# Optimization experiments

Hardware: AMD Instinct MI355X
Metric: run time of the kernel (lower is better)

The kernel has to match this reference:

```python
import jax, jax.numpy as jnp
import numpy as np

B, V, T, D, NC = 512, 4, 16, 512, 174
EPS = 1e-5
_edges = np.ones((V, V)) - np.eye(V)
SEND = np.where(_edges)[0]   # [12]
RECV = np.where(_edges)[1]   # [12]
E2N = jnp.asarray(np.eye(V)[RECV].T, dtype=jnp.float32)  # [V, E] one-hot recv matrix


def _bn(x, g, b):
    # BatchNorm1d in training mode: batch stats over flattened rows, biased var
    m = x.mean(axis=0)
    v = jnp.var(x, axis=0)
    return (x - m) * jax.lax.rsqrt(v + EPS) * g + b


def _mlp(x, w1, b1, w2, b2, g, bb):
    # RefNRIMLP: Linear-ELU-(Dropout p=0.1 disabled/eval)-Linear-ELU-BN
    h = jax.nn.elu(x @ w1 + b1)
    h = jax.nn.elu(h @ w2 + b2)
    return _bn(h, g, bb)


def setup_inputs() -> dict:
    key = jax.random.key(0)
    ks = iter(jax.random.split(key, 64))
    def W(*s):
        return jax.random.normal(next(ks), s, dtype=jnp.float32) * 0.02
    def zeros(*s):
        return jnp.zeros(s, jnp.float32)
    def ones(*s):
        return jnp.ones(s, jnp.float32)
    return dict(
        global_img_input=zeros(1),
        box_categories=jax.random.randint(next(ks), (B, T, V), 0, 3),
        box_input=jax.random.uniform(next(ks), (B, T, V, 4), dtype=jnp.float32),
        hand_id=jax.random.randint(next(ks), (B,), 0, 2),
        video_label=jax.random.randint(next(ks), (B,), 0, NC),
        emb=W(3, D // 2),
        c2f_w1=W(4, D // 2), c2f_g1=ones(D // 2), c2f_b1=zeros(D // 2),
        c2f_w2=W(D // 2, D), c2f_g2=ones(D), c2f_b2=zeros(D),
        fus_w=W(D + D // 2, D), fus_g=ones(D), fus_b=zeros(D),
        m1_w1=W(2 * D, D), m1_b1=zeros(D), m1_w2=W(D, D), m1_b2=zeros(D), m1_g=ones(D), m1_bb=zeros(D),
        m2_w1=W(D, D), m2_b1=zeros(D), m2_w2=W(D, D), m2_b2=zeros(D), m2_g=ones(D), m2_bb=zeros(D),
        t1_w1=W(2 * D, D), t1_b1=zeros(D), t1_w2=W(D, D), t1_b2=zeros(D), t1_g=ones(D), t1_bb=zeros(D),
        ps_w1=W(D, D), ps_g1=ones(D), ps_b1=zeros(D), ps_w2=W(D, D), ps_g2=ones(D), ps_b2=zeros(D),
        tb_w1=W(T * D, D), tb_g1=ones(D), tb_b1=zeros(D), tb_w2=W(D, D), tb_g2=ones(D), tb_b2=zeros(D),
        cl_w1=W(D, D), cl_b1=zeros(D), cl_w2=W(D, 512), cl_b2=zeros(512),
        cl_w3=W(512, NC), cl_b3=zeros(NC),
    )


def reference(global_img_input, box_categories, box_input, hand_id, video_label,
              emb, c2f_w1, c2f_g1, c2f_b1, c2f_w2, c2f_g2, c2f_b2,
              fus_w, fus_g, fus_b,
              m1_w1, m1_b1, m1_w2, m1_b2, m1_g, m1_bb,
              m2_w1, m2_b1, m2_w2, m2_b2, m2_g, m2_bb,
              t1_w1, t1_b1, t1_w2, t1_b2, t1_g, t1_bb,
              ps_w1, ps_g1, ps_b1, ps_w2, ps_g2, ps_b2,
              tb_w1, tb_g1, tb_b1, tb_w2, tb_g2, tb_b2,
              cl_w1, cl_b1, cl_w2, cl_b2, cl_w3, cl_b3):
    b = hand_id.shape[0]
    # [b,T,V,*] -> [b,V,T,*] -> flatten rows
    x = box_input.transpose(0, 2, 1, 3).reshape(-1, 4)          # [b*V*T, 4]
    cats = box_categories.transpose(0, 2, 1).reshape(-1)        # [b*V*T]
    pad_mask = (jnp.arange(3)[:, None] != 0).astype(emb.dtype)  # padding_idx=0
    ce = (emb * pad_mask)[cats]                                 # [b*V*T, D/2]
    # coord_to_feature: Linear(no bias)-BN-ReLU x2
    h = jax.nn.relu(_bn(x @ c2f_w1, c2f_g1, c2f_b1))
    h = jax.nn.relu(_bn(h @ c2f_w2, c2f_g2, c2f_b2))
    # coord_category_fusion
    bf = jax.nn.relu(_bn(jnp.concatenate([h, ce], axis=1) @ fus_w, fus_g, fus_b))
    bf = bf.reshape(b, V, T, D)
    # node2edge gather + mlp1
    e = jnp.concatenate([bf[:, SEND], bf[:, RECV]], axis=-1).reshape(-1, 2 * D)
    e = _mlp(e, m1_w1, m1_b1, m1_w2, m1_b2, m1_g, m1_bb).reshape(b, len(SEND), T, D)
    # edge2node: one-hot matmul aggregation / (V-1)
    n = jnp.einsum('ve,betd->bvtd', E2N, e) / (V - 1)
    n = _mlp(n.reshape(-1, D), m2_w1, m2_b1, m2_w2, m2_b2, m2_g, m2_bb).reshape(b, V, T, D)
    # temporal MLP on cat(node, bf)
    p = jnp.concatenate([n, bf], axis=-1).reshape(-1, 2 * D)
    p = _mlp(p, t1_w1, t1_b1, t1_w2, t1_b2, t1_g, t1_bb)
    # point_spatial_node_fusion
    p = jax.nn.relu(_bn(p @ ps_w1, ps_g1, ps_b1))
    p = jax.nn.relu(_bn(p @ ps_w2, ps_g2, ps_b2))
    # t_box_feature_fusion over flattened time
    q = p.reshape(b * V, T * D)
    q = jax.nn.relu(_bn(q @ tb_w1, tb_g1, tb_b1))
    q = jax.nn.relu(_bn(q @ tb_w2, tb_g2, tb_b2))
    feat = q.reshape(b, V, D).mean(axis=1)                      # mean over boxes
    h1 = jax.nn.relu(feat @ cl_w1 + cl_b1)
    h2 = jax.nn.relu(h1 @ cl_w2 + cl_b2)
    pf = h2 @ cl_w3 + cl_b3                                      # [b, NC]
    return (pf, video_label)
```

## Files before the change

kernel.cpp:

```cpp
#include <hip/hip_runtime.h>
#include <math.h>

#define EPS_ 1e-5f

static constexpr int Bb = 512, Vv = 4, Tt = 16, Dd = 512, NCc = 174;
static constexpr int NROW = Bb * Vv * Tt;
static constexpr int EROW = Bb * 12 * Tt;
static constexpr int CB = 128;
static constexpr int NCHUNK = Bb / CB;
static constexpr int CROWS_N = CB * Vv * Tt;
static constexpr int CROWS_E = CB * 12 * Tt;

__constant__ int d_SEND[12] = {0,0,0,1,1,1,2,2,2,3,3,3};
__constant__ int d_RECV[12] = {1,2,3,0,2,3,0,1,3,0,1,2};
__constant__ int d_EOFV[4][3] = {{3,6,9},{0,7,10},{1,4,11},{2,5,8}};

typedef float f32x4 __attribute__((ext_vector_type(4)));
typedef short s16x8 __attribute__((ext_vector_type(8)));

static __device__ __forceinline__ float b2f(unsigned short u) {
    union { unsigned int i; float f; } x; x.i = ((unsigned int)u) << 16; return x.f;
}
static __device__ __forceinline__ unsigned short f2b(float f) {
    union { float f; unsigned int i; } x; x.f = f;
    unsigned int r = (x.i + 0x7fffu + ((x.i >> 16) & 1u)) >> 16;
    return (unsigned short)r;
}
static __device__ __forceinline__ float act_f(float v, int act) {
    if (act == 1) return fmaxf(v, 0.f);
    if (act == 2) return (v > 0.f) ? v : (__expf(v) - 1.f);
    return v;
}

#define GL2LDS(g, l) __builtin_amdgcn_global_load_lds(                     \
    (__attribute__((address_space(1))) void*)(g),                          \
    (__attribute__((address_space(3))) void*)(l), 16, 0, 0)

#define CS_STRIDE 136

__global__ __launch_bounds__(256) void gemm_bf16(
    const unsigned short* __restrict__ A0, int Ka0, int K0,
    const unsigned short* __restrict__ A1, int Ka1, int K1,
    const unsigned short* __restrict__ WT, int Kw, int wtoff,
    unsigned short* __restrict__ C, int M, int N,
    const float* __restrict__ bias, int act,
    float* __restrict__ pstats, int accum,
    float* __restrict__ Cpart, int Ksl)
{
    __shared__ __align__(16) unsigned short SMEM[128 * CS_STRIDE];
    unsigned short* SA0 = SMEM;
    unsigned short* SB0 = SMEM + 4096;
    unsigned short* SA1 = SMEM + 8192;
    unsigned short* SB1 = SMEM + 12288;
    int tid = threadIdx.x;
    int lane = tid & 63, wave = tid >> 6;
    int wr = wave >> 1, wc = wave & 1;
    int g = lane >> 4, r16 = lane & 15;

    int nct = N >> 7, nrt = M >> 7;
    int id = blockIdx.x, bx, by;
    if ((nrt & 7) == 0) {
        int grp = id / (nct * 8);
        int rem = id - grp * nct * 8;
        by = grp * 8 + (rem & 7);
        bx = rem >> 3;
    } else { bx = id % nct; by = id / nct; }
    int rowBase = by * 128;
    int colBase = bx * 128;
    int koff = blockIdx.z * Ksl;

    int srow = wave * 32 + (lane >> 2);
    int scol = (lane & 3) * 8;
    const unsigned short* wrow  = WT + (size_t)(colBase + srow) * Kw + wtoff + scol;
    const unsigned short* wrow2 = WT + (size_t)(colBase + srow + 16) * Kw + wtoff + scol;

    f32x4 acc[4][4];
#pragma unroll
    for (int i = 0; i < 4; ++i)
#pragma unroll
        for (int j = 0; j < 4; ++j) acc[i][j] = (f32x4){0.f, 0.f, 0.f, 0.f};

#define STAGE_(kg_, SA_, SB_) do {                                              \
        int kg = (kg_);                                                         \
        const unsigned short* Ap; int lda; int kc;                              \
        if (kg < K0) { Ap = A0; lda = Ka0; kc = kg; }                           \
        else         { Ap = A1; lda = Ka1; kc = kg - K0; }                      \
        const unsigned short* ga = Ap + (size_t)(rowBase + srow) * lda + kc + scol; \
        GL2LDS(ga, (SA_) + wave * 1024);                                        \
        GL2LDS(ga + (size_t)16 * lda, (SA_) + wave * 1024 + 512);               \
        GL2LDS(wrow + kg, (SB_) + wave * 1024);                                 \
        GL2LDS(wrow2 + kg, (SB_) + wave * 1024 + 512);                          \
    } while (0)

    int nt = Ksl >> 5;
    STAGE_(koff, SA0, SB0);
    __syncthreads();
    for (int t = 0; t < nt; ++t) {
        unsigned short* SA = (t & 1) ? SA1 : SA0;
        unsigned short* SB = (t & 1) ? SB1 : SB0;
        if (t + 1 < nt) {
            unsigned short* PA = (t & 1) ? SA0 : SA1;
            unsigned short* PB = (t & 1) ? SB0 : SB1;
            STAGE_(koff + (t + 1) * 32, PA, PB);
        }
        s16x8 xf[4], wf[4];
#pragma unroll
        for (int j = 0; j < 4; ++j)
            xf[j] = *(const s16x8*)(SA + (wr * 64 + j * 16 + r16) * 32 + g * 8);
#pragma unroll
        for (int i = 0; i < 4; ++i)
            wf[i] = *(const s16x8*)(SB + (wc * 64 + i * 16 + r16) * 32 + g * 8);
#pragma unroll
        for (int i = 0; i < 4; ++i)
#pragma unroll
            for (int j = 0; j < 4; ++j)
                acc[i][j] = __builtin_amdgcn_mfma_f32_16x16x32_bf16(
                    wf[i], xf[j], acc[i][j], 0, 0, 0);
        __syncthreads();
    }
#undef STAGE_

    if (Cpart) {
#pragma unroll
        for (int j = 0; j < 4; ++j) {
            int row = rowBase + wr * 64 + j * 16 + r16;
#pragma unroll
            for (int i = 0; i < 4; ++i) {
                int col0 = colBase + wc * 64 + i * 16 + g * 4;
                float4 v = make_float4(acc[i][j][0], acc[i][j][1],
                                       acc[i][j][2], acc[i][j][3]);
                *(float4*)&Cpart[((size_t)blockIdx.z * M + row) * N + col0] = v;
            }
        }
        return;
    }

#pragma unroll
    for (int i = 0; i < 4; ++i) {
        int lc0 = wc * 64 + i * 16 + g * 4;
        float4 b4 = bias ? *(const float4*)(bias + colBase + lc0)
                         : make_float4(0.f, 0.f, 0.f, 0.f);
        float s[4] = {0.f, 0.f, 0.f, 0.f}, q[4] = {0.f, 0.f, 0.f, 0.f};
#pragma unroll
        for (int j = 0; j < 4; ++j) {
            int lr = wr * 64 + j * 16 + r16;
            float v0 = act_f(acc[i][j][0] + b4.x, act);
            float v1 = act_f(acc[i][j][1] + b4.y, act);
            float v2 = act_f(acc[i][j][2] + b4.z, act);
            float v3 = act_f(acc[i][j][3] + b4.w, act);
            *(ushort4*)&SMEM[lr * CS_STRIDE + lc0] =
                make_ushort4(f2b(v0), f2b(v1), f2b(v2), f2b(v3));
            s[0] += v0; s[1] += v1; s[2] += v2; s[3] += v3;
            q[0] += v0 * v0; q[1] += v1 * v1; q[2] += v2 * v2; q[3] += v3 * v3;
        }
        if (pstats) {
#pragma unroll
            for (int p = 0; p < 4; ++p) {
#pragma unroll
                for (int d = 1; d < 16; d <<= 1) {
                    s[p] += __shfl_xor(s[p], d);
                    q[p] += __shfl_xor(q[p], d);
                }
            }
            if (r16 == 0) {
                float* pr = pstats + ((size_t)(by * 2 + wr)) * 1024 + colBase + lc0;
                float4 s4 = make_float4(s[0], s[1], s[2], s[3]);
                float4 q4 = make_float4(q[0], q[1], q[2], q[3]);
                if (accum) {
                    float4 o = *(float4*)pr;
                    s4.x += o.x; s4.y += o.y; s4.z += o.z; s4.w += o.w;
                    float4 o2 = *(float4*)(pr + 512);
                    q4.x += o2.x; q4.y += o2.y; q4.z += o2.z; q4.w += o2.w;
                }
                *(float4*)pr = s4;
                *(float4*)(pr + 512) = q4;
            }
        }
    }
    __syncthreads();
    {
        int qd = tid & 3;
        int rr = tid >> 2;
#pragma unroll
        for (int pass = 0; pass < 2; ++pass) {
            int lr = pass * 64 + rr;
            size_t grow = (size_t)(rowBase + lr) * N + colBase;
#pragma unroll
            for (int u = 0; u < 4; ++u) {
                int cofs = u * 32 + qd * 8;
                uint4 v = *(const uint4*)(SMEM + lr * CS_STRIDE + cofs);
                *(uint4*)&C[grow + cofs] = v;
            }
        }
    }
}

__global__ __launch_bounds__(256) void finalize_stats_k(
    const float* __restrict__ P, int nrows, float* __restrict__ slot)
{
    __shared__ float red[256];
    int lane = threadIdx.x & 63;
    int seg  = threadIdx.x >> 6;
    int col  = blockIdx.x * 64 + lane;
    float s = 0.f;
    for (int r = seg; r < nrows; r += 4)
        s += P[(size_t)r * 1024 + col];
    red[threadIdx.x] = s;
    __syncthreads();
    if (seg == 0)
        slot[col] = red[lane] + red[64 + lane] + red[128 + lane] + red[192 + lane];
}

__global__ __launch_bounds__(256) void combine_k(
    const float4* __restrict__ P, int S, int M,
    unsigned short* __restrict__ C, float* __restrict__ pstats, int act)
{
    int col4 = threadIdx.x & 127;
    int rh = threadIdx.x >> 7;
    int rb = blockIdx.y * 8;
    float4 s4 = make_float4(0.f, 0.f, 0.f, 0.f);
    float4 q4 = make_float4(0.f, 0.f, 0.f, 0.f);
#pragma unroll
    for (int i = 0; i < 4; ++i) {
        int row = rb + rh + 2 * i;
        float4 v = make_float4(0.f, 0.f, 0.f, 0.f);
#pragma unroll
        for (int z = 0; z < 8; ++z) {
            float4 p = P[((size_t)z * M + row) * 128 + col4];
            v.x += p.x; v.y += p.y; v.z += p.z; v.w += p.w;
        }
        v.x = act_f(v.x, act); v.y = act_f(v.y, act);
        v.z = act_f(v.z, act); v.w = act_f(v.w, act);
        ((ushort4*)C)[(size_t)row * 128 + col4] =
            make_ushort4(f2b(v.x), f2b(v.y), f2b(v.z), f2b(v.w));
        s4.x += v.x; s4.y += v.y; s4.z += v.z; s4.w += v.w;
        q4.x += v.x * v.x; q4.y += v.y * v.y; q4.z += v.z * v.z; q4.w += v.w * v.w;
    }
    __shared__ float4 sb[256], qb[256];
    sb[threadIdx.x] = s4; qb[threadIdx.x] = q4;
    __syncthreads();
    if (threadIdx.x < 128) {
        float4 a = sb[threadIdx.x], b = sb[threadIdx.x + 128];
        float4 c = qb[threadIdx.x], d = qb[threadIdx.x + 128];
        int col = threadIdx.x * 4;
        float* pr = pstats + (size_t)blockIdx.y * 1024 + col;
        *(float4*)pr = make_float4(a.x + b.x, a.y + b.y, a.z + b.z, a.w + b.w);
        *(float4*)(pr + 512) = make_float4(c.x + d.x, c.y + d.y, c.z + d.z, c.w + d.w);
    }
}

#define NTD 13
struct TBatch {
    const float* src[NTD];
    unsigned short* dst[NTD];
    int K[NTD];
    long base[NTD + 1];
};
__global__ __launch_bounds__(256) void transpose_batch_k(TBatch tb, long total)
{
    long i = (long)blockIdx.x * 256 + threadIdx.x;
    if (i >= total) return;
    int d = 0;
#pragma unroll
    for (int j = 0; j < NTD; ++j) if (i >= tb.base[j + 1]) d = j + 1;
    long r = i - tb.base[d];
    int k = (int)(r >> 9), n = (int)(r & 511);
    tb.dst[d][(size_t)n * tb.K[d] + k] = f2b(tb.src[d][r]);
}

__global__ __launch_bounds__(256) void transpose_pq_k(
    const float* __restrict__ W, unsigned short* __restrict__ WT)
{
    int i = blockIdx.x * 256 + threadIdx.x;
    if (i >= 512 * 1024) return;
    int k = i >> 10, n = i & 1023;
    float v = (n < 512) ? W[(size_t)k * 512 + n] : W[(size_t)(512 + k) * 512 + (n - 512)];
    WT[(size_t)n * 512 + k] = f2b(v);
}

__global__ __launch_bounds__(256) void colstats_k(
    const unsigned short* __restrict__ X, float* __restrict__ P)
{
    __shared__ float sb[256][4], qb[256][4];
    int c4 = threadIdx.x & 63;
    int seg = threadIdx.x >> 6;
    int r0 = blockIdx.x * 128;
    float s[4] = {0.f, 0.f, 0.f, 0.f}, q[4] = {0.f, 0.f, 0.f, 0.f};
    for (int r = r0 + seg; r < r0 + 128; r += 4) {
        ushort4 x = ((const ushort4*)X)[(size_t)r * 64 + c4];
        float v0 = b2f(x.x), v1 = b2f(x.y), v2 = b2f(x.z), v3 = b2f(x.w);
        s[0] += v0; s[1] += v1; s[2] += v2; s[3] += v3;
        q[0] += v0 * v0; q[1] += v1 * v1; q[2] += v2 * v2; q[3] += v3 * v3;
    }
#pragma unroll
    for (int e = 0; e < 4; ++e) { sb[threadIdx.x][e] = s[e]; qb[threadIdx.x][e] = q[e]; }
    __syncthreads();
    if (threadIdx.x < 64) {
        int c = threadIdx.x;
        float4 S, Q;
        S.x = sb[c][0] + sb[c + 64][0] + sb[c + 128][0] + sb[c + 192][0];
        S.y = sb[c][1] + sb[c + 64][1] + sb[c + 128][1] + sb[c + 192][1];
        S.z = sb[c][2] + sb[c + 64][2] + sb[c + 128][2] + sb[c + 192][2];
        S.w = sb[c][3] + sb[c + 64][3] + sb[c + 128][3] + sb[c + 192][3];
        Q.x = qb[c][0] + qb[c + 64][0] + qb[c + 128][0] + qb[c + 192][0];
        Q.y = qb[c][1] + qb[c + 64][1] + qb[c + 128][1] + qb[c + 192][1];
        Q.z = qb[c][2] + qb[c + 64][2] + qb[c + 128][2] + qb[c + 192][2];
        Q.w = qb[c][3] + qb[c + 64][3] + qb[c + 128][3] + qb[c + 192][3];
        *(float4*)&P[(size_t)blockIdx.x * 1024 + c * 4] = S;
        *(float4*)&P[(size_t)blockIdx.x * 1024 + 512 + c * 4] = Q;
    }
}

__global__ __launch_bounds__(256) void bn_apply_k(
    unsigned short* __restrict__ X, long n4, int cmask4, int C,
    const float* __restrict__ slot, const float* __restrict__ gm,
    const float* __restrict__ bt, float inv_cnt, float premul, int act)
{
    __shared__ float sc_s[512], sh_s[512];
    for (int c = threadIdx.x; c < C; c += 256) {
        float mean = slot[c] * inv_cnt;
        float var = fmaxf(slot[512 + c] * inv_cnt - mean * mean, 0.f);
        float sc = gm[c] * rsqrtf(var + EPS_);
        sc_s[c] = sc * premul;
        sh_s[c] = bt[c] - mean * sc;
    }
    __syncthreads();
    long stride = (long)gridDim.x * 256;
    for (long i = (long)blockIdx.x * 256 + threadIdx.x; i < n4; i += stride) {
        ushort4 x = ((ushort4*)X)[i];
        int c = ((int)(i & cmask4)) * 4;
        unsigned short o[4] = {x.x, x.y, x.z, x.w};
#pragma unroll
        for (int e = 0; e < 4; ++e) {
            float v = b2f(o[e]) * sc_s[c + e] + sh_s[c + e];
            o[e] = f2b(act_f(v, act));
        }
        ((ushort4*)X)[i] = make_ushort4(o[0], o[1], o[2], o[3]);
    }
}

__global__ __launch_bounds__(256) void zero_k(float* p, int n)
{
    int i = blockIdx.x * 256 + threadIdx.x;
    if (i < n) p[i] = 0.f;
}

__global__ __launch_bounds__(256) void build_x0_k(
    const float* __restrict__ box, float* __restrict__ X0)
{
    int i = blockIdx.x * 256 + threadIdx.x;
    if (i >= NROW * 4) return;
    int c = i & 3; int r = i >> 2;
    int t = r & 15; int bv = r >> 4; int v = bv & 3; int b = bv >> 2;
    X0[i] = box[(((size_t)b * Tt + t) * Vv + v) * 4 + c];
}

__global__ __launch_bounds__(256) void build_ce_k(
    const int* __restrict__ cats, const float* __restrict__ emb,
    unsigned short* __restrict__ CE)
{
    int i = blockIdx.x * 256 + threadIdx.x;
    if (i >= NROW * 64) return;
    int c4 = i & 63; int r = i >> 6;
    int t = r & 15; int bv = r >> 4; int v = bv & 3; int b = bv >> 2;
    int cat = cats[((size_t)b * Tt + t) * Vv + v];
    unsigned short o[4];
#pragma unroll
    for (int e = 0; e < 4; ++e)
        o[e] = (cat == 0) ? 0 : f2b(emb[cat * 256 + c4 * 4 + e]);
    ((ushort4*)CE)[(size_t)r * 64 + c4] = make_ushort4(o[0], o[1], o[2], o[3]);
}

__global__ __launch_bounds__(256) void smallk_gemm_k(
    const float* __restrict__ X0, const float* __restrict__ W4,
    unsigned short* __restrict__ Y1)
{
    int i = blockIdx.x * 256 + threadIdx.x;
    if (i >= NROW * 64) return;
    int n4 = i & 63; int m = i >> 6;
    float4 x = *(const float4*)(X0 + m * 4);
    unsigned short o[4];
#pragma unroll
    for (int e = 0; e < 4; ++e) {
        int n = n4 * 4 + e;
        float v = x.x * W4[n] + x.y * W4[256 + n] + x.z * W4[512 + n] + x.w * W4[768 + n];
        o[e] = f2b(v);
    }
    ((ushort4*)Y1)[(size_t)m * 64 + n4] = make_ushort4(o[0], o[1], o[2], o[3]);
}

__global__ __launch_bounds__(256) void edge_gather_k(
    const unsigned short* __restrict__ PQ,
    const float* __restrict__ b1, unsigned short* __restrict__ E)
{
    int i = blockIdx.x * 256 + threadIdx.x;
    if (i >= CROWS_E * 128) return;
    int c4 = i & 127; int m = i >> 7;
    int t = m & 15; int be = m >> 4; int e = be % 12; int brel = be / 12;
    int s = d_SEND[e], r = d_RECV[e];
    ushort4 p = ((const ushort4*)PQ)[(((size_t)brel * 4 + s) * 16 + t) * 256 + c4];
    ushort4 q = ((const ushort4*)PQ)[(((size_t)brel * 4 + r) * 16 + t) * 256 + 128 + c4];
    unsigned short pa[4] = {p.x, p.y, p.z, p.w}, qa[4] = {q.x, q.y, q.z, q.w}, o[4];
#pragma unroll
    for (int e2 = 0; e2 < 4; ++e2) {
        float v = b2f(pa[e2]) + b2f(qa[e2]) + b1[c4 * 4 + e2];
        o[e2] = f2b(act_f(v, 2));
    }
    ((ushort4*)E)[i] = make_ushort4(o[0], o[1], o[2], o[3]);
}

__global__ __launch_bounds__(256) void edge_agg_k(
    const unsigned short* __restrict__ E2c, unsigned short* __restrict__ nraw, int b0)
{
    int i = blockIdx.x * 256 + threadIdx.x;
    if (i >= CB * Vv * Tt * 128) return;
    int c4 = i & 127; int r = i >> 7;
    int t = r & 15; int r2 = r >> 4; int v = r2 & 3; int brel = r2 >> 2;
    float s[4] = {0.f, 0.f, 0.f, 0.f};
#pragma unroll
    for (int j = 0; j < 3; ++j) {
        int e = d_EOFV[v][j];
        ushort4 x = ((const ushort4*)E2c)[(((size_t)brel * 12 + e) * 16 + t) * 128 + c4];
        s[0] += b2f(x.x); s[1] += b2f(x.y); s[2] += b2f(x.z); s[3] += b2f(x.w);
    }
    ((ushort4*)nraw)[((((size_t)(b0 + brel)) * 4 + v) * 16 + t) * 128 + c4] =
        make_ushort4(f2b(s[0]), f2b(s[1]), f2b(s[2]), f2b(s[3]));
}

__global__ __launch_bounds__(256) void feat_mean_k(
    const unsigned short* __restrict__ q, unsigned short* __restrict__ feat)
{
    int i = blockIdx.x * 256 + threadIdx.x;
    if (i >= Bb * 128) return;
    int c4 = i & 127; int b = i >> 7;
    float s[4] = {0.f, 0.f, 0.f, 0.f};
#pragma unroll
    for (int v = 0; v < 4; ++v) {
        ushort4 x = ((const ushort4*)q)[(((size_t)b * 4 + v)) * 128 + c4];
        s[0] += b2f(x.x); s[1] += b2f(x.y); s[2] += b2f(x.z); s[3] += b2f(x.w);
    }
    ((ushort4*)feat)[(size_t)b * 128 + c4] = make_ushort4(
        f2b(0.25f * s[0]), f2b(0.25f * s[1]), f2b(0.25f * s[2]), f2b(0.25f * s[3]));
}

__global__ __launch_bounds__(256) void final_gemm_k(
    const unsigned short* __restrict__ H2, const float* __restrict__ W,
    const float* __restrict__ b, float* __restrict__ out)
{
    int i = blockIdx.x * 256 + threadIdx.x;
    if (i >= Bb * NCc) return;
    int n = i % NCc; int m = i / NCc;
    float s = b[n];
    for (int k = 0; k < 512; ++k)
        s += b2f(H2[(size_t)m * 512 + k]) * W[(size_t)k * NCc + n];
    out[i] = s;
}

__global__ __launch_bounds__(256) void copy_labels_k(
    const int* __restrict__ lab, float* __restrict__ out)
{
    int i = blockIdx.x * 256 + threadIdx.x;
    if (i < Bb) out[i] = (float)lab[i];
}

static inline void gemm(hipStream_t s,
                        const unsigned short* A0, int Ka0, int K0,
                        const unsigned short* A1, int Ka1, int K1,
                        const unsigned short* WT, int Kw, int wtoff,
                        unsigned short* C, int M, int N,
                        const float* bias, int act, float* pstats, int accum)
{
    dim3 g((N / 128) * (M / 128), 1, 1);
    hipLaunchKernelGGL(gemm_bf16, g, dim3(256), 0, s,
                       A0, Ka0, K0, A1, Ka1, K1, WT, Kw, wtoff, C, M, N,
                       bias, act, pstats, accum, (float*)nullptr, K0 + K1);
}

static inline void finalize(hipStream_t s, const float* P, int nrows, float* slot)
{
    hipLaunchKernelGGL(finalize_stats_k, dim3(16), dim3(256), 0, s, P, nrows, slot);
}

static inline void bn_apply(hipStream_t s, unsigned short* X, long n, int C,
                            const float* slot, const float* gm, const float* bt,
                            float cnt, float premul, int act)
{
    long n4 = n / 4;
    long nb = (n4 + 255) / 256;
    if (nb > 1024) nb = 1024;
    hipLaunchKernelGGL(bn_apply_k, dim3((unsigned)nb), dim3(256), 0, s,
                       X, n4, C / 4 - 1, C, slot, gm, bt, 1.f / cnt, premul, act);
}

extern "C" void kernel_launch(void* const* d_in, const int* in_sizes, int n_in,
                              void* d_out, int out_size, void* d_ws, size_t ws_size,
                              hipStream_t stream)
{
    const int*   box_cat = (const int*)  d_in[1];
    const float* box_in  = (const float*)d_in[2];
    const int*   vlabel  = (const int*)  d_in[4];
    const float* emb     = (const float*)d_in[5];
    const float* c2f_w1  = (const float*)d_in[6];
    const float* c2f_g1  = (const float*)d_in[7];
    const float* c2f_b1  = (const float*)d_in[8];
    const float* c2f_w2  = (const float*)d_in[9];
    const float* c2f_g2  = (const float*)d_in[10];
    const float* c2f_b2  = (const float*)d_in[11];
    const float* fus_w   = (const float*)d_in[12];
    const float* fus_g   = (const float*)d_in[13];
    const float* fus_b   = (const float*)d_in[14];
    const float* m1_w1   = (const float*)d_in[15];
    const float* m1_b1   = (const float*)d_in[16];
    const float* m1_w2   = (const float*)d_in[17];
    const float* m1_b2   = (const float*)d_in[18];
    const float* m1_g    = (const float*)d_in[19];
    const float* m1_bb   = (const float*)d_in[20];
    const float* m2_w1   = (const float*)d_in[21];
    const float* m2_b1   = (const float*)d_in[22];
    const float* m2_w2   = (const float*)d_in[23];
    const float* m2_b2   = (const float*)d_in[24];
    const float* m2_g    = (const float*)d_in[25];
    const float* m2_bb   = (const float*)d_in[26];
    const float* t1_w1   = (const float*)d_in[27];
    const float* t1_b1   = (const float*)d_in[28];
    const float* t1_w2   = (const float*)d_in[29];
    const float* t1_b2   = (const float*)d_in[30];
    const float* t1_g    = (const float*)d_in[31];
    const float* t1_bb   = (const float*)d_in[32];
    const float* ps_w1   = (const float*)d_in[33];
    const float* ps_g1   = (const float*)d_in[34];
    const float* ps_b1   = (const float*)d_in[35];
    const float* ps_w2   = (const float*)d_in[36];
    const float* ps_g2   = (const float*)d_in[37];
    const float* ps_b2   = (const float*)d_in[38];
    const float* tb_w1   = (const float*)d_in[39];
    const float* tb_g1   = (const float*)d_in[40];
    const float* tb_b1   = (const float*)d_in[41];
    const float* tb_w2   = (const float*)d_in[42];
    const float* tb_g2   = (const float*)d_in[43];
    const float* tb_b2   = (const float*)d_in[44];
    const float* cl_w1   = (const float*)d_in[45];
    const float* cl_b1   = (const float*)d_in[46];
    const float* cl_w2   = (const float*)d_in[47];
    const float* cl_b2   = (const float*)d_in[48];
    const float* cl_w3   = (const float*)d_in[49];
    const float* cl_b3   = (const float*)d_in[50];

    float* out = (float*)d_out;

    char* base = (char*)d_ws;
    const size_t SZ_ACT = (size_t)NROW * 512 * 2;
    unsigned short* A0v = (unsigned short*)(base);
    unsigned short* A1v = (unsigned short*)(base + SZ_ACT);
    char* Sreg = base + 2 * SZ_ACT;
    unsigned short* A2v = (unsigned short*)Sreg;
    unsigned short* CE  = (unsigned short*)Sreg;
    unsigned short* Y1  = (unsigned short*)(Sreg + (size_t)NROW * 256 * 2);
    unsigned short* PQc = (unsigned short*)Sreg;
    unsigned short* EC1 = (unsigned short*)(Sreg + (size_t)CROWS_N * 1024 * 2);
    unsigned short* EC2 = (unsigned short*)(Sreg + (size_t)CROWS_N * 1024 * 2
                                                 + (size_t)CROWS_E * 512 * 2);
    float* Ppart = (float*)Sreg;
    char* wtb = Sreg + (size_t)CROWS_N * 1024 * 2 + 2 * (size_t)CROWS_E * 512 * 2;
    unsigned short* wtp = (unsigned short*)wtb;
    size_t wo = 0;
    auto alloc_wt = [&](int K) { unsigned short* p = wtp + wo; wo += (size_t)K * 512; return p; };
    unsigned short* WTc2f2 = alloc_wt(256);
    unsigned short* WTfus  = alloc_wt(768);
    unsigned short* WTpq   = alloc_wt(1024);
    unsigned short* WTm1b  = alloc_wt(512);
    unsigned short* WTm2a  = alloc_wt(512);
    unsigned short* WTm2b  = alloc_wt(512);
    unsigned short* WTt1a  = alloc_wt(1024);
    unsigned short* WTt1b  = alloc_wt(512);
    unsigned short* WTps1  = alloc_wt(512);
    unsigned short* WTps2  = alloc_wt(512);
    unsigned short* WTtb1  = alloc_wt(8192);
    unsigned short* WTtb2  = alloc_wt(512);
    unsigned short* WTcl1  = alloc_wt(512);
    unsigned short* WTcl2  = alloc_wt(512);
    float* X0f    = (float*)(wtp + wo);
    float* STATS  = X0f + (size_t)NROW * 4;
    float* PSTATS = STATS + 10 * 1024;

    auto slot = [&](int i) { return STATS + (size_t)i * 1024; };

    {
        int nz = 10 * 1024 + 384 * 1024;
        hipLaunchKernelGGL(zero_k, dim3((nz + 255) / 256), dim3(256), 0, stream,
                           STATS, nz);
    }
    {
        TBatch tb;
        const float* srcs[NTD] = {c2f_w2, fus_w, m1_w2, m2_w1, m2_w2, t1_w1, t1_w2,
                                  ps_w1, ps_w2, tb_w1, tb_w2, cl_w1, cl_w2};
        unsigned short* dsts[NTD] = {WTc2f2, WTfus, WTm1b, WTm2a, WTm2b, WTt1a, WTt1b,
                                     WTps1, WTps2, WTtb1, WTtb2, WTcl1, WTcl2};
        int Ks[NTD] = {256, 768, 512, 512, 512, 1024, 512, 512, 512, 8192, 512, 512, 512};
        long acc = 0;
        for (int i = 0; i < NTD; ++i) {
            tb.src[i] = srcs[i]; tb.dst[i] = dsts[i]; tb.K[i] = Ks[i];
            tb.base[i] = acc; acc += (long)Ks[i] * 512;
        }
        tb.base[NTD] = acc;
        hipLaunchKernelGGL(transpose_batch_k, dim3((unsigned)((acc + 255) / 256)),
                           dim3(256), 0, stream, tb, acc);
    }
    hipLaunchKernelGGL(transpose_pq_k, dim3((512 * 1024 + 255) / 256), dim3(256), 0,
                       stream, m1_w1, WTpq);

    hipLaunchKernelGGL(build_x0_k, dim3((NROW * 4 + 255) / 256), dim3(256), 0, stream,
                       box_in, X0f);
    hipLaunchKernelGGL(build_ce_k, dim3((NROW * 64 + 255) / 256), dim3(256), 0, stream,
                       box_cat, emb, CE);

    hipLaunchKernelGGL(smallk_gemm_k, dim3((NROW * 64 + 255) / 256), dim3(256), 0,
                       stream, X0f, c2f_w1, Y1);
    hipLaunchKernelGGL(colstats_k, dim3(NROW / 128), dim3(256), 0, stream, Y1, PSTATS);
    finalize(stream, PSTATS, NROW / 128, slot(0));
    bn_apply(stream, Y1, (long)NROW * 256, 256, slot(0), c2f_g1, c2f_b1,
             (float)NROW, 1.f, 1);

    gemm(stream, Y1, 256, 256, nullptr, 0, 0, WTc2f2, 256, 0, A1v, NROW, 512,
         nullptr, 0, PSTATS, 0);
    finalize(stream, PSTATS, 512, slot(1));
    bn_apply(stream, A1v, (long)NROW * 512, 512, slot(1), c2f_g2, c2f_b2,
             (float)NROW, 1.f, 1);

    gemm(stream, A1v, 512, 512, CE, 256, 256, WTfus, 768, 0, A0v, NROW, 512,
         nullptr, 0, PSTATS, 0);
    finalize(stream, PSTATS, 512, slot(2));
    bn_apply(stream, A0v, (long)NROW * 512, 512, slot(2), fus_g, fus_b,
             (float)NROW, 1.f, 1);

    for (int c = 0; c < NCHUNK; ++c) {
        const unsigned short* BFc = A0v + (size_t)c * CROWS_N * 512;
        gemm(stream, BFc, 512, 512, nullptr, 0, 0, WTpq, 512, 0, PQc, CROWS_N, 1024,
             nullptr, 0, nullptr, 0);
        hipLaunchKernelGGL(edge_gather_k, dim3((CROWS_E * 128 + 255) / 256), dim3(256),
                           0, stream, PQc, m1_b1, EC1);
        gemm(stream, EC1, 512, 512, nullptr, 0, 0, WTm1b, 512, 0, EC2, CROWS_E, 512,
             m1_b2, 2, PSTATS, 1);
        hipLaunchKernelGGL(edge_agg_k, dim3((CB * Vv * Tt * 128 + 255) / 256), dim3(256),
                           0, stream, EC2, A1v, c * CB);
    }
    finalize(stream, PSTATS, 384, slot(3));
    bn_apply(stream, A1v, (long)NROW * 512, 512, slot(3), m1_g, m1_bb,
             (float)EROW, 1.f / 3.f, 0);

    gemm(stream, A1v, 512, 512, nullptr, 0, 0, WTm2a, 512, 0, A2v, NROW, 512,
         m2_b1, 2, nullptr, 0);
    gemm(stream, A2v, 512, 512, nullptr, 0, 0, WTm2b, 512, 0, A1v, NROW, 512,
         m2_b2, 2, PSTATS, 0);
    finalize(stream, PSTATS, 512, slot(4));
    bn_apply(stream, A1v, (long)NROW * 512, 512, slot(4), m2_g, m2_bb,
             (float)NROW, 1.f, 0);

    gemm(stream, A1v, 512, 512, A0v, 512, 512, WTt1a, 1024, 0, A2v, NROW, 512,
         t1_b1, 2, nullptr, 0);
    gemm(stream, A2v, 512, 512, nullptr, 0, 0, WTt1b, 512, 0, A1v, NROW, 512,
         t1_b2, 2, PSTATS, 0);
    finalize(stream, PSTATS, 512, slot(5));
    bn_apply(stream, A1v, (long)NROW * 512, 512, slot(5), t1_g, t1_bb,
             (float)NROW, 1.f, 0);

    gemm(stream, A1v, 512, 512, nullptr, 0, 0, WTps1, 512, 0, A2v, NROW, 512,
         nullptr, 0, PSTATS, 0);
    finalize(stream, PSTATS, 512, slot(6));
    bn_apply(stream, A2v, (long)NROW * 512, 512, slot(6), ps_g1, ps_b1,
             (float)NROW, 1.f, 1);

    gemm(stream, A2v, 512, 512, nullptr, 0, 0, WTps2, 512, 0, A0v, NROW, 512,
         nullptr, 0, PSTATS, 0);
    finalize(stream, PSTATS, 512, slot(7));
    bn_apply(stream, A0v, (long)NROW * 512, 512, slot(7), ps_g2, ps_b2,
             (float)NROW, 1.f, 1);

    {
        dim3 g((512 / 128) * (2048 / 128), 1, 8);
        hipLaunchKernelGGL(gemm_bf16, g, dim3(256), 0, stream,
                           A0v, 8192, 8192, (const unsigned short*)nullptr, 0, 0,
                           WTtb1, 8192, 0, A1v, 2048, 512,
                           (const float*)nullptr, 0, (float*)nullptr, 0, Ppart, 1024);
        hipLaunchKernelGGL(combine_k, dim3(1, 2048 / 8), dim3(256), 0, stream,
                           (const float4*)Ppart, 8, 2048, A1v, PSTATS, 0);
        finalize(stream, PSTATS, 2048 / 8, slot(8));
    }
    bn_apply(stream, A1v, (long)Bb * Vv * 512, 512, slot(8), tb_g1, tb_b1,
             (float)(Bb * Vv), 1.f, 1);

    gemm(stream, A1v, 512, 512, nullptr, 0, 0, WTtb2, 512, 0, A2v, Bb * Vv, 512,
         nullptr, 0, PSTATS, 0);
    finalize(stream, PSTATS, (Bb * Vv / 128) * 2, slot(9));
    bn_apply(stream, A2v, (long)Bb * Vv * 512, 512, slot(9), tb_g2, tb_b2,
             (float)(Bb * Vv), 1.f, 1);

    hipLaunchKernelGGL(feat_mean_k, dim3((Bb * 128 + 255) / 256), dim3(256), 0, stream,
                       A2v, A0v);

    gemm(stream, A0v, 512, 512, nullptr, 0, 0, WTcl1, 512, 0, A1v, Bb, 512,
         cl_b1, 1, nullptr, 0);
    gemm(stream, A1v, 512, 512, nullptr, 0, 0, WTcl2, 512, 0, A2v, Bb, 512,
         cl_b2, 1, nullptr, 0);
    hipLaunchKernelGGL(final_gemm_k, dim3((Bb * NCc + 255) / 256), dim3(256), 0, stream,
                       A2v, cl_w3, cl_b3, out);

    hipLaunchKernelGGL(copy_labels_k, dim3((Bb + 255) / 256), dim3(256), 0, stream,
                       vlabel, out + (size_t)Bb * NCc);
}
```

Before: 1.335 ms.

## Triple-buffer GEMM LDS pipeline and tile weight transposes through LDS

The bf16 GEMM now uses three LDS stages, prefetching two K-tiles ahead. It waits with explicit vmcnt counts and one barrier per iteration instead of two syncthreads, so global loads overlap more with MFMA work. The weight-transpose kernels now stage 64x64 tiles in shared memory, making both reads and writes coalesced. The risks are higher LDS use, which may reduce occupancy, and reliance on exact vmcnt accounting for correctness.

```diff
diff --git a/kernel.cpp b/kernel.cpp
--- a/kernel.cpp
+++ b/kernel.cpp
@@ -47,11 +47,7 @@
     float* __restrict__ pstats, int accum,
     float* __restrict__ Cpart, int Ksl)
 {
-    __shared__ __align__(16) unsigned short SMEM[128 * CS_STRIDE];
-    unsigned short* SA0 = SMEM;
-    unsigned short* SB0 = SMEM + 4096;
-    unsigned short* SA1 = SMEM + 8192;
-    unsigned short* SB1 = SMEM + 12288;
+    __shared__ __align__(16) unsigned short SMEM[24576];
     int tid = threadIdx.x;
     int lane = tid & 63, wave = tid >> 6;
     int wr = wave >> 1, wc = wave & 1;
@@ -80,29 +76,33 @@
 #pragma unroll
         for (int j = 0; j < 4; ++j) acc[i][j] = (f32x4){0.f, 0.f, 0.f, 0.f};
 
-#define STAGE_(kg_, SA_, SB_) do {                                              \
+#define STAGE_(kg_, SL_) do {                                                   \
         int kg = (kg_);                                                         \
         const unsigned short* Ap; int lda; int kc;                              \
         if (kg < K0) { Ap = A0; lda = Ka0; kc = kg; }                           \
         else         { Ap = A1; lda = Ka1; kc = kg - K0; }                      \
         const unsigned short* ga = Ap + (size_t)(rowBase + srow) * lda + kc + scol; \
-        GL2LDS(ga, (SA_) + wave * 1024);                                        \
-        GL2LDS(ga + (size_t)16 * lda, (SA_) + wave * 1024 + 512);               \
-        GL2LDS(wrow + kg, (SB_) + wave * 1024);                                 \
-        GL2LDS(wrow2 + kg, (SB_) + wave * 1024 + 512);                          \
+        GL2LDS(ga, (SL_) + wave * 1024);                                        \
+        GL2LDS(ga + (size_t)16 * lda, (SL_) + wave * 1024 + 512);               \
+        GL2LDS(wrow + kg, (SL_) + 4096 + wave * 1024);                          \
+        GL2LDS(wrow2 + kg, (SL_) + 4096 + wave * 1024 + 512);                   \
     } while (0)
 
     int nt = Ksl >> 5;
-    STAGE_(koff, SA0, SB0);
-    __syncthreads();
+    STAGE_(koff, SMEM);
+    if (nt > 1) STAGE_(koff + 32, SMEM + 8192);
+    int cur = 0;
     for (int t = 0; t < nt; ++t) {
-        unsigned short* SA = (t & 1) ? SA1 : SA0;
-        unsigned short* SB = (t & 1) ? SB1 : SB0;
-        if (t + 1 < nt) {
-            unsigned short* PA = (t & 1) ? SA0 : SA1;
-            unsigned short* PB = (t & 1) ? SB0 : SB1;
-            STAGE_(koff + (t + 1) * 32, PA, PB);
+        if (t + 1 < nt) asm volatile("s_waitcnt vmcnt(4)" ::: "memory");
+        else            asm volatile("s_waitcnt vmcnt(0)" ::: "memory");
+        __builtin_amdgcn_s_barrier();
+        __builtin_amdgcn_sched_barrier(0);
+        if (t + 2 < nt) {
+            int nx = cur + 2; if (nx >= 3) nx -= 3;
+            STAGE_(koff + (t + 2) * 32, SMEM + nx * 8192);
         }
+        unsigned short* SA = SMEM + cur * 8192;
+        unsigned short* SB = SA + 4096;
         s16x8 xf[4], wf[4];
 #pragma unroll
         for (int j = 0; j < 4; ++j)
@@ -116,9 +116,10 @@
             for (int j = 0; j < 4; ++j)
                 acc[i][j] = __builtin_amdgcn_mfma_f32_16x16x32_bf16(
                     wf[i], xf[j], acc[i][j], 0, 0, 0);
-        __syncthreads();
+        cur = (cur == 2) ? 0 : cur + 1;
     }
 #undef STAGE_
+    __syncthreads();
 
     if (Cpart) {
 #pragma unroll
@@ -254,28 +255,58 @@
     const float* src[NTD];
     unsigned short* dst[NTD];
     int K[NTD];
-    long base[NTD + 1];
+    int tbase[NTD + 1];
 };
-__global__ __launch_bounds__(256) void transpose_batch_k(TBatch tb, long total)
-{
-    long i = (long)blockIdx.x * 256 + threadIdx.x;
-    if (i >= total) return;
+__global__ __launch_bounds__(256) void transpose_batch_k(TBatch tb)
+{
+    int id = blockIdx.x;
     int d = 0;
 #pragma unroll
-    for (int j = 0; j < NTD; ++j) if (i >= tb.base[j + 1]) d = j + 1;
-    long r = i - tb.base[d];
-    int k = (int)(r >> 9), n = (int)(r & 511);
-    tb.dst[d][(size_t)n * tb.K[d] + k] = f2b(tb.src[d][r]);
+    for (int j = 0; j < NTD; ++j) if (id >= tb.tbase[j + 1]) d = j + 1;
+    int rel = id - tb.tbase[d];
+    int kt = rel >> 3, ntl = rel & 7;
+    int k0 = kt * 64, n0 = ntl * 64;
+    const float* S = tb.src[d];
+    unsigned short* D = tb.dst[d];
+    int K = tb.K[d];
+    __shared__ unsigned short L[64][68];
+    int c = threadIdx.x & 63;
+    int r = threadIdx.x >> 6;
+#pragma unroll
+    for (int p = 0; p < 16; ++p) {
+        int kk = r + p * 4;
+        L[kk][c] = f2b(S[(size_t)(k0 + kk) * 512 + n0 + c]);
+    }
+    __syncthreads();
+#pragma unroll
+    for (int p = 0; p < 16; ++p) {
+        int nn = r + p * 4;
+        D[(size_t)(n0 + nn) * K + k0 + c] = L[c][nn];
+    }
 }
 
 __global__ __launch_bounds__(256) void transpose_pq_k(
     const float* __restrict__ W, unsigned short* __restrict__ WT)
 {
-    int i = blockIdx.x * 256 + threadIdx.x;
-    if (i >= 512 * 1024) return;
-    int k = i >> 10, n = i & 1023;
-    float v = (n < 512) ? W[(size_t)k * 512 + n] : W[(size_t)(512 + k) * 512 + (n - 512)];
-    WT[(size_t)n * 512 + k] = f2b(v);
+    int id = blockIdx.x;
+    int kt = id >> 4, ntl = id & 15;
+    int k0 = kt * 64, n0 = ntl * 64;
+    __shared__ unsigned short L[64][68];
+    int c = threadIdx.x & 63;
+    int r = threadIdx.x >> 6;
+    int nb = n0 + c;
+    const float* S = (n0 < 512) ? (W + nb) : (W + (size_t)512 * 512 + (nb - 512));
+#pragma unroll
+    for (int p = 0; p < 16; ++p) {
+        int kk = r + p * 4;
+        L[kk][c] = f2b(S[(size_t)(k0 + kk) * 512]);
+    }
+    __syncthreads();
+#pragma unroll
+    for (int p = 0; p < 16; ++p) {
+        int nn = r + p * 4;
+        WT[(size_t)(n0 + nn) * 512 + k0 + c] = L[c][nn];
+    }
 }
 
 __global__ __launch_bounds__(256) void colstats_k(
@@ -597,17 +628,16 @@
         unsigned short* dsts[NTD] = {WTc2f2, WTfus, WTm1b, WTm2a, WTm2b, WTt1a, WTt1b,
                                      WTps1, WTps2, WTtb1, WTtb2, WTcl1, WTcl2};
         int Ks[NTD] = {256, 768, 512, 512, 512, 1024, 512, 512, 512, 8192, 512, 512, 512};
-        long acc = 0;
+        int acc = 0;
         for (int i = 0; i < NTD; ++i) {
             tb.src[i] = srcs[i]; tb.dst[i] = dsts[i]; tb.K[i] = Ks[i];
-            tb.base[i] = acc; acc += (long)Ks[i] * 512;
+            tb.tbase[i] = acc; acc += (Ks[i] / 64) * 8;
         }
-        tb.base[NTD] = acc;
-        hipLaunchKernelGGL(transpose_batch_k, dim3((unsigned)((acc + 255) / 256)),
-                           dim3(256), 0, stream, tb, acc);
-    }
-    hipLaunchKernelGGL(transpose_pq_k, dim3((512 * 1024 + 255) / 256), dim3(256), 0,
-                       stream, m1_w1, WTpq);
+        tb.tbase[NTD] = acc;
+        hipLaunchKernelGGL(transpose_batch_k, dim3((unsigned)acc), dim3(256), 0,
+                           stream, tb);
+    }
+    hipLaunchKernelGGL(transpose_pq_k, dim3(128), dim3(256), 0, stream, m1_w1, WTpq);
 
     hipLaunchKernelGGL(build_x0_k, dim3((NROW * 4 + 255) / 256), dim3(256), 0, stream,
                        box_in, X0f);
```

New measurement: 1.275 ms. 1.05x faster.
